# Optimization experiments

Hardware: AMD Instinct MI355X
Metric: run time of the kernel (lower is better)

## Reference

```python
import jax, jax.numpy as jnp
import numpy as np

DIM = 1024
DIM_HEAD = 64
HEADS = 8
INNER = DIM_HEAD * HEADS
EPS = 1e-5


def layernorm(x, g, b):
    mu = jnp.mean(x, axis=-1, keepdims=True)
    var = jnp.var(x, axis=-1, keepdims=True)
    return (x - mu) * jax.lax.rsqrt(var + EPS) * g + b


def setup_inputs() -> dict:
    key = jax.random.key(0)
    ks = jax.random.split(key, 8)
    b, n, m = 8, 4096, 64
    x = jax.random.normal(ks[0], (b, n, DIM), dtype=jnp.float32)
    latents = jax.random.normal(ks[1], (b, m, DIM), dtype=jnp.float32)
    mask = jax.random.bernoulli(ks[2], 0.9, (b, n))
    s = DIM ** -0.5
    Wq = jax.random.normal(ks[3], (DIM, INNER), dtype=jnp.float32) * s
    Wkv = jax.random.normal(ks[4], (DIM, 2 * INNER), dtype=jnp.float32) * s
    Wo = jax.random.normal(ks[5], (INNER, DIM), dtype=jnp.float32) * (INNER ** -0.5)
    ln_x_g = jnp.ones((DIM,), jnp.float32); ln_x_b = jnp.zeros((DIM,), jnp.float32)
    ln_l_g = jnp.ones((DIM,), jnp.float32); ln_l_b = jnp.zeros((DIM,), jnp.float32)
    ln_o_g = jnp.ones((DIM,), jnp.float32); ln_o_b = jnp.zeros((DIM,), jnp.float32)
    return {"x": x, "latents": latents, "mask": mask,
            "Wq": Wq, "Wkv": Wkv, "Wo": Wo,
            "ln_x_g": ln_x_g, "ln_x_b": ln_x_b,
            "ln_l_g": ln_l_g, "ln_l_b": ln_l_b,
            "ln_o_g": ln_o_g, "ln_o_b": ln_o_b}


def reference(x, latents, mask, Wq, Wkv, Wo, ln_x_g, ln_x_b, ln_l_g, ln_l_b, ln_o_g, ln_o_b):
    scale = DIM_HEAD ** -0.5
    b, m = latents.shape[0], latents.shape[1]
    xn = layernorm(x, ln_x_g, ln_x_b)
    ln = layernorm(latents, ln_l_g, ln_l_b)
    q = ln @ Wq                                   # [b, m, inner]
    kv_in = jnp.concatenate([xn, ln], axis=1)     # [b, n+m, dim]
    kv = kv_in @ Wkv                              # [b, n+m, 2*inner]
    k, v = jnp.split(kv, 2, axis=-1)
    # b n (h d) -> b h n d
    q = q.reshape(b, m, HEADS, DIM_HEAD).transpose(0, 2, 1, 3)
    k = k.reshape(b, k.shape[1], HEADS, DIM_HEAD).transpose(0, 2, 1, 3)
    v = v.reshape(b, v.shape[1], HEADS, DIM_HEAD).transpose(0, 2, 1, 3)
    # NOTE: scale applied twice, faithful to the original module.
    sim = jnp.einsum('bhid,bhjd->bhij', q * scale, k) * scale
    full_mask = jnp.concatenate([mask, jnp.ones((b, m), dtype=bool)], axis=1)  # pad True for latents
    max_neg = -jnp.finfo(sim.dtype).max
    sim = jnp.where(full_mask[:, None, None, :], sim, max_neg)
    attn = jax.nn.softmax(sim.astype(jnp.float32), axis=-1).astype(sim.dtype)
    out = jnp.einsum('bhij,bhjd->bhid', attn, v)
    out = out.transpose(0, 2, 1, 3).reshape(b, m, INNER)
    out = out @ Wo
    return layernorm(out, ln_o_g, ln_o_b)
```

## Files before the change

### kernel.cpp

```cpp
#include <hip/hip_runtime.h>

typedef unsigned short u16;
typedef unsigned int u32;
using f32x4  = __attribute__((ext_vector_type(4))) float;
using short8 = __attribute__((ext_vector_type(8))) short;
using s16x4  = __attribute__((ext_vector_type(4))) short;
using u16x4  = __attribute__((ext_vector_type(4))) unsigned short;

#define DEV __device__ __forceinline__

DEV u16 f2bf(float f) {
  u32 u = __float_as_uint(f);
  u32 r = u + 0x7fffu + ((u >> 16) & 1u);
  return (u16)(r >> 16);
}

DEV void gload_lds16(const void* g, void* l) {
  __builtin_amdgcn_global_load_lds(
      (__attribute__((address_space(1))) void*)g,
      (__attribute__((address_space(3))) void*)l, 16, 0, 0);
}

DEV void block_reduce2(float& a, float& b, float* red) {
#pragma unroll
  for (int m = 1; m < 64; m <<= 1) {
    a += __shfl_xor(a, m);
    b += __shfl_xor(b, m);
  }
  const int wid = threadIdx.x >> 6, lane = threadIdx.x & 63;
  __syncthreads();
  if (lane == 0) { red[wid] = a; red[4 + wid] = b; }
  __syncthreads();
  a = red[0] + red[1] + red[2] + red[3];
  b = red[4] + red[5] + red[6] + red[7];
}

__global__ __launch_bounds__(256) void ln_rows_k(
    const float* __restrict__ X, const float* __restrict__ g,
    const float* __restrict__ be, u16* __restrict__ out, int mode)
{
  __shared__ float red[8];
  const int r = blockIdx.x, t = threadIdx.x;
  const float4 v = *(const float4*)(X + (((size_t)r) << 10) + t * 4);
  float s1 = v.x + v.y + v.z + v.w;
  float s2 = v.x * v.x + v.y * v.y + v.z * v.z + v.w * v.w;
  block_reduce2(s1, s2, red);
  const float mean = s1 * (1.f / 1024.f);
  const float var  = s2 * (1.f / 1024.f) - mean * mean;
  const float rstd = rsqrtf(var + 1e-5f);
  const float4 gv = *(const float4*)(g + t * 4);
  const float4 bv = *(const float4*)(be + t * 4);
  u16x4 o;
  o[0] = f2bf((v.x - mean) * rstd * gv.x + bv.x);
  o[1] = f2bf((v.y - mean) * rstd * gv.y + bv.y);
  o[2] = f2bf((v.z - mean) * rstd * gv.z + bv.z);
  o[3] = f2bf((v.w - mean) * rstd * gv.w + bv.w);
  const size_t orow = (mode == 0)
      ? ((size_t)(r >> 12) * 4160 + (r & 4095))
      : ((size_t)(r >> 6) * 4160 + 4096 + (r & 63));
  *(u16x4*)(out + orow * 1024 + t * 4) = o;
}

__global__ __launch_bounds__(256) void transpose_w_k(
    const float* __restrict__ W, u16* __restrict__ Wt, int K, int N)
{
  __shared__ float tile[32][33];
  const int n0 = blockIdx.x * 32, k0 = blockIdx.y * 32;
  const int tx = threadIdx.x, ty = threadIdx.y;
#pragma unroll
  for (int i = 0; i < 4; ++i)
    tile[ty + 8 * i][tx] = W[(size_t)(k0 + ty + 8 * i) * N + n0 + tx];
  __syncthreads();
#pragma unroll
  for (int i = 0; i < 4; ++i)
    Wt[(size_t)(n0 + ty + 8 * i) * K + k0 + tx] = f2bf(tile[tx][ty + 8 * i]);
}

__global__ __launch_bounds__(256) void mask_bias_k(const void* __restrict__ mask,
                                                   float* __restrict__ bias)
{
  __shared__ int flag_s;
  if (threadIdx.x == 0) {
    const u32* mw = (const u32*)mask;
    bool fpat = true, ipat = true;
    for (int i = 0; i < 256; ++i) {
      u32 w = mw[i];
      if (w != 0u && w != 0x3f800000u) fpat = false;
      if (w > 1u) ipat = false;
    }
    flag_s = fpat ? 2 : (ipat ? 1 : 0);
  }
  __syncthreads();
  const int flag = flag_s;
  const int idx = blockIdx.x * 256 + threadIdx.x;
  const int b = idx / 4160, j = idx - b * 4160;
  float bv = 0.f;
  if (j < 4096) {
    const int mi = b * 4096 + j;
    bool on;
    if (flag == 2)      on = ((const float*)mask)[mi] != 0.f;
    else if (flag == 1) on = ((const int*)mask)[mi] != 0;
    else                on = ((const unsigned char*)mask)[mi] != 0;
    bv = on ? 0.f : -1e30f;
  }
  bias[idx] = bv;
}

__global__ __launch_bounds__(512, 4) void gemm2_k(
    const u16* __restrict__ xnl, const u16* __restrict__ Wq_t,
    const u16* __restrict__ Wkv_t,
    u16* __restrict__ q_h, u16* __restrict__ k_h, u16* __restrict__ v_t)
{
  __shared__ __attribute__((aligned(16))) short As[3][4096];
  __shared__ __attribute__((aligned(16))) short Bs[3][8192];

  const int tid = threadIdx.x, lane = tid & 63;
  const int wid = tid >> 6, wr = wid >> 2, wc = wid & 3;
  const int l15 = lane & 15, lq = lane >> 4;

  const int bid = blockIdx.x;
  int mode, mblk, nblk;
  const u16 *Ap, *Bp;
  if (bid < 520)       { mode = 0; mblk = bid % 260; nblk = bid / 260; Ap = xnl; Bp = Wkv_t; }
  else if (bid < 1040) { const int r2 = bid - 520; mode = 2; mblk = r2 & 3; nblk = r2 >> 2;
                         Ap = Wkv_t + (size_t)512 * 1024; Bp = xnl; }
  else                 { const int r2 = bid - 1040; mode = 1; mblk = r2 >> 1; nblk = r2 & 1;
                         Ap = xnl; Bp = Wq_t; }
  const int m0 = mblk * 128, n0 = nblk * 256;

  const int srow = tid >> 2, sslot = tid & 3;
  const u32 ss = (u32)((sslot ^ ((srow >> 1) & 3)) * 8);
  const int gra = m0 + srow;
  const u32 arow = (mode == 1) ? ((u32)(gra >> 6) * 4160u + 4096u + (u32)(gra & 63)) : (u32)gra;
  const u32 aoff  = arow * 1024u + ss;
  const u32 boff0 = (u32)(n0 + srow) * 1024u + ss;
  const u32 boff1 = (u32)(n0 + 128 + srow) * 1024u + ss;

  const int rsw = ((lq ^ ((l15 >> 1) & 3)) << 4);
  const int aRd = wr * 4096 + l15 * 64 + rsw;
  const int bRd = wc * 4096 + l15 * 64 + rsw;

  const f32x4 z4 = {0.f, 0.f, 0.f, 0.f};
  f32x4 acc[4][4];
#pragma unroll
  for (int i = 0; i < 4; ++i)
#pragma unroll
    for (int j = 0; j < 4; ++j) acc[i][j] = z4;

  auto stage = [&](int buf, int T) {
    gload_lds16(Ap + aoff  + (u32)T * 32u, &As[buf][tid * 8]);
    gload_lds16(Bp + boff0 + (u32)T * 32u, &Bs[buf][tid * 8]);
    gload_lds16(Bp + boff1 + (u32)T * 32u, &Bs[buf][4096 + tid * 8]);
  };

  stage(0, 0);
  stage(1, 1);
  asm volatile("s_waitcnt vmcnt(3)" ::: "memory");
  __builtin_amdgcn_s_barrier();

  int c0 = 0, c1 = 1, c2 = 2;
#pragma unroll 1
  for (int t = 0; t < 32; ++t) {
    if (t < 30) stage(c2, t + 2);
    const char* aB = (const char*)&As[0][0] + c0 * 8192  + aRd;
    const char* bB = (const char*)&Bs[0][0] + c0 * 16384 + bRd;
    short8 af[4], bf[4];
#pragma unroll
    for (int mi = 0; mi < 4; ++mi) af[mi] = *(const short8*)(aB + mi * 1024);
#pragma unroll
    for (int nj = 0; nj < 4; ++nj) bf[nj] = *(const short8*)(bB + nj * 1024);
    __builtin_amdgcn_s_setprio(1);
#pragma unroll
    for (int mi = 0; mi < 4; ++mi)
#pragma unroll
      for (int nj = 0; nj < 4; ++nj)
        acc[mi][nj] = __builtin_amdgcn_mfma_f32_16x16x32_bf16(af[mi], bf[nj], acc[mi][nj], 0, 0, 0);
    __builtin_amdgcn_s_setprio(0);
    if (t < 30)       { asm volatile("s_waitcnt vmcnt(3)" ::: "memory"); }
    else if (t == 30) { asm volatile("s_waitcnt vmcnt(0)" ::: "memory"); }
    __builtin_amdgcn_s_barrier();
    const int tmp = c0; c0 = c1; c1 = c2; c2 = tmp;
  }

#pragma unroll
  for (int mi = 0; mi < 4; ++mi)
#pragma unroll
    for (int nj = 0; nj < 4; ++nj)
#pragma unroll
      for (int r = 0; r < 4; ++r) {
        const int gm = m0 + wr * 64 + mi * 16 + lq * 4 + r;
        const int gn = n0 + wc * 64 + nj * 16 + l15;
        const u16 v = f2bf(acc[mi][nj][r]);
        if (mode == 0) {
          const int b = gm / 4160, j = gm - b * 4160;
          k_h[(((size_t)b * 8 + (gn >> 6)) * 4160 + j) * 64 + (gn & 63)] = v;
        } else if (mode == 2) {
          const int b = gn / 4160, j = gn - b * 4160;
          v_t[(((size_t)b * 8 + (gm >> 6)) * 64 + (gm & 63)) * 4160 + j] = v;
        } else {
          const int b = gm >> 6, i2 = gm & 63;
          q_h[(((size_t)b * 8 + (gn >> 6)) * 64 + i2) * 64 + (gn & 63)] = v;
        }
      }
}

__global__ __launch_bounds__(256) void attn_k(
    const u16* __restrict__ q_h, const u16* __restrict__ k_h,
    const u16* __restrict__ v_t, const float* __restrict__ bias,
    float* __restrict__ O_part, float* __restrict__ m_part,
    float* __restrict__ l_part)
{
  __shared__ __attribute__((aligned(16))) short Ks[4096];
  __shared__ __attribute__((aligned(16))) short Vs[4096];
  __shared__ __attribute__((aligned(16))) short Ps[4][1152];
  __shared__ float biasS[64];
  const int bid = blockIdx.x;
  const int sp = bid & 7, bh = bid >> 3;
  const int b = bh >> 3;
  const int tid = threadIdx.x, wid = tid >> 6, lane = tid & 63;
  const int t0 = sp ? (8 * sp + 1) : 0;
  const int tc = sp ? 8 : 9;

  const size_t qoff = ((size_t)bh * 64 + wid * 16 + (lane & 15)) * 64 + 8 * (lane >> 4);
  const short8 qf0 = *(const short8*)&q_h[qoff];
  const short8 qf1 = *(const short8*)&q_h[qoff + 32];

  float mrun = -1e30f, lrun = 0.f;
  const f32x4 z4 = {0.f, 0.f, 0.f, 0.f};
  f32x4 o[4] = {z4, z4, z4, z4};
  const size_t khead = (size_t)bh * (4160 * 64);
  const size_t vhead = (size_t)bh * (64 * 4160);

  for (int tt = 0; tt < tc; ++tt) {
    const int t = t0 + tt;
#pragma unroll
    for (int p = 0; p < 2; ++p) {
      const int lo = (p * 256 + tid) * 16;
      const int row = lo >> 7;
      const int src = lo ^ ((row & 7) << 4);
      gload_lds16((const char*)k_h + (khead + (size_t)t * 4096) * 2 + src,
                  (char*)Ks + (p * 256 + wid * 64) * 16);
    }
#pragma unroll
    for (int p = 0; p < 2; ++p) {
      const int lo = (p * 256 + tid) * 16;
      const int row = lo >> 7;
      const int colb = (lo ^ ((row & 7) << 4)) & 127;
      gload_lds16((const char*)v_t + (vhead + (size_t)row * 4160 + t * 64) * 2 + colb,
                  (char*)Vs + (p * 256 + wid * 64) * 16);
    }
    if (tid < 64) biasS[tid] = bias[b * 4160 + t * 64 + tid];
    __syncthreads();

    f32x4 sc[4] = {z4, z4, z4, z4};
#pragma unroll
    for (int mi = 0; mi < 4; ++mi) {
      const int row = mi * 16 + (lane & 15);
      const int sw = (row & 7) << 4;
      short8 a0 = *(const short8*)((const char*)Ks + ((row * 128 + 16 * (lane >> 4)) ^ sw));
      sc[mi] = __builtin_amdgcn_mfma_f32_16x16x32_bf16(a0, qf0, sc[mi], 0, 0, 0);
      short8 a1 = *(const short8*)((const char*)Ks + ((row * 128 + 64 + 16 * (lane >> 4)) ^ sw));
      sc[mi] = __builtin_amdgcn_mfma_f32_16x16x32_bf16(a1, qf1, sc[mi], 0, 0, 0);
    }

    float sv[4][4];
    float tmax = -3e30f;
#pragma unroll
    for (int mi = 0; mi < 4; ++mi)
#pragma unroll
      for (int r = 0; r < 4; ++r) {
        const int kv = mi * 16 + (lane >> 4) * 4 + r;
        const float s = sc[mi][r] * (1.f / 64.f) + biasS[kv];
        sv[mi][r] = s;
        tmax = fmaxf(tmax, s);
      }
    tmax = fmaxf(tmax, __shfl_xor(tmax, 16));
    tmax = fmaxf(tmax, __shfl_xor(tmax, 32));
    const float mnew = fmaxf(mrun, tmax);
    const float fac = __expf(mrun - mnew);
    float psum = 0.f;
#pragma unroll
    for (int mi = 0; mi < 4; ++mi) {
      s16x4 pk;
#pragma unroll
      for (int r = 0; r < 4; ++r) {
        const float p = __expf(sv[mi][r] - mnew);
        psum += p;
        pk[r] = (short)f2bf(p);
      }
      *(s16x4*)&Ps[wid][(lane & 15) * 72 + mi * 16 + (lane >> 4) * 4] = pk;
    }
    psum += __shfl_xor(psum, 16);
    psum += __shfl_xor(psum, 32);
    lrun = lrun * fac + psum;
    mrun = mnew;
#pragma unroll
    for (int mi = 0; mi < 4; ++mi)
#pragma unroll
      for (int e = 0; e < 4; ++e) o[mi][e] *= fac;

#pragma unroll
    for (int mi = 0; mi < 4; ++mi) {
      const int row = mi * 16 + (lane & 15);
      const int sw = (row & 7) << 4;
      short8 a0 = *(const short8*)((const char*)Vs + ((row * 128 + 16 * (lane >> 4)) ^ sw));
      short8 p0 = *(const short8*)&Ps[wid][(lane & 15) * 72 + 8 * (lane >> 4)];
      o[mi] = __builtin_amdgcn_mfma_f32_16x16x32_bf16(a0, p0, o[mi], 0, 0, 0);
      short8 a1 = *(const short8*)((const char*)Vs + ((row * 128 + 64 + 16 * (lane >> 4)) ^ sw));
      short8 p1 = *(const short8*)&Ps[wid][(lane & 15) * 72 + 32 + 8 * (lane >> 4)];
      o[mi] = __builtin_amdgcn_mfma_f32_16x16x32_bf16(a1, p1, o[mi], 0, 0, 0);
    }
    __syncthreads();
  }

#pragma unroll
  for (int mi = 0; mi < 4; ++mi)
#pragma unroll
    for (int r = 0; r < 4; ++r) {
      const int d = mi * 16 + (lane >> 4) * 4 + r;
      const int q = wid * 16 + (lane & 15);
      O_part[(((size_t)sp * 64 + bh) * 64 + d) * 64 + q] = o[mi][r];
    }
  if (lane < 16) {
    m_part[((size_t)sp * 64 + bh) * 64 + wid * 16 + lane] = mrun;
    l_part[((size_t)sp * 64 + bh) * 64 + wid * 16 + lane] = lrun;
  }
}

__global__ __launch_bounds__(256) void combine_k(
    const float* __restrict__ O_part, const float* __restrict__ m_part,
    const float* __restrict__ l_part, float* __restrict__ attn_out)
{
  __shared__ float wgt[8][64];
  const int bh = blockIdx.x;
  const int b = bh >> 3, h = bh & 7;
  const int t = threadIdx.x;
  if (t < 64) {
    float mv[8], lv[8];
#pragma unroll
    for (int s = 0; s < 8; ++s) {
      mv[s] = m_part[((size_t)s * 64 + bh) * 64 + t];
      lv[s] = l_part[((size_t)s * 64 + bh) * 64 + t];
    }
    float M = mv[0];
#pragma unroll
    for (int s = 1; s < 8; ++s) M = fmaxf(M, mv[s]);
    float den = 0.f;
#pragma unroll
    for (int s = 0; s < 8; ++s) den += lv[s] * __expf(mv[s] - M);
    const float inv = 1.f / den;
#pragma unroll
    for (int s = 0; s < 8; ++s) wgt[s][t] = __expf(mv[s] - M) * inv;
  }
  __syncthreads();
#pragma unroll
  for (int i = 0; i < 16; ++i) {
    const int p = i * 256 + t;
    const int d = p >> 6, q = p & 63;
    float acc = 0.f;
#pragma unroll
    for (int s = 0; s < 8; ++s)
      acc += O_part[(((size_t)s * 64 + bh) * 64 + d) * 64 + q] * wgt[s][q];
    attn_out[((size_t)b * 64 + q) * 512 + h * 64 + d] = acc;
  }
}

__global__ __launch_bounds__(256) void outproj_k(
    const float* __restrict__ attn_out, const float* __restrict__ Wo,
    const float* __restrict__ g, const float* __restrict__ be,
    float* __restrict__ out)
{
  __shared__ float arow[2][512];
  __shared__ float red[8];
  const int rb = blockIdx.x * 2, t = threadIdx.x;
  arow[0][t]       = attn_out[(size_t)rb * 512 + t];
  arow[0][t + 256] = attn_out[(size_t)rb * 512 + 256 + t];
  arow[1][t]       = attn_out[(size_t)(rb + 1) * 512 + t];
  arow[1][t + 256] = attn_out[(size_t)(rb + 1) * 512 + 256 + t];
  __syncthreads();
  float a0x = 0, a0y = 0, a0z = 0, a0w = 0;
  float a1x = 0, a1y = 0, a1z = 0, a1w = 0;
  for (int k = 0; k < 512; ++k) {
    const float4 w = *(const float4*)(Wo + (size_t)k * 1024 + t * 4);
    const float x0 = arow[0][k], x1 = arow[1][k];
    a0x += x0 * w.x; a0y += x0 * w.y; a0z += x0 * w.z; a0w += x0 * w.w;
    a1x += x1 * w.x; a1y += x1 * w.y; a1z += x1 * w.z; a1w += x1 * w.w;
  }
  const float4 gv = *(const float4*)(g + t * 4);
  const float4 bv = *(const float4*)(be + t * 4);
  {
    float s1 = a0x + a0y + a0z + a0w;
    float s2 = a0x * a0x + a0y * a0y + a0z * a0z + a0w * a0w;
    block_reduce2(s1, s2, red);
    const float mean = s1 * (1.f / 1024.f);
    const float rstd = rsqrtf(s2 * (1.f / 1024.f) - mean * mean + 1e-5f);
    float4 ov;
    ov.x = (a0x - mean) * rstd * gv.x + bv.x;
    ov.y = (a0y - mean) * rstd * gv.y + bv.y;
    ov.z = (a0z - mean) * rstd * gv.z + bv.z;
    ov.w = (a0w - mean) * rstd * gv.w + bv.w;
    *(float4*)(out + (size_t)rb * 1024 + t * 4) = ov;
  }
  {
    float s1 = a1x + a1y + a1z + a1w;
    float s2 = a1x * a1x + a1y * a1y + a1z * a1z + a1w * a1w;
    block_reduce2(s1, s2, red);
    const float mean = s1 * (1.f / 1024.f);
    const float rstd = rsqrtf(s2 * (1.f / 1024.f) - mean * mean + 1e-5f);
    float4 ov;
    ov.x = (a1x - mean) * rstd * gv.x + bv.x;
    ov.y = (a1y - mean) * rstd * gv.y + bv.y;
    ov.z = (a1z - mean) * rstd * gv.z + bv.z;
    ov.w = (a1w - mean) * rstd * gv.w + bv.w;
    *(float4*)(out + (size_t)(rb + 1) * 1024 + t * 4) = ov;
  }
}

extern "C" void kernel_launch(void* const* d_in, const int* in_sizes, int n_in,
                              void* d_out, int out_size, void* d_ws, size_t ws_size,
                              hipStream_t stream) {
  (void)in_sizes; (void)n_in; (void)out_size; (void)ws_size;
  const float* x       = (const float*)d_in[0];
  const float* latents = (const float*)d_in[1];
  const void*  mask    = d_in[2];
  const float* Wq      = (const float*)d_in[3];
  const float* Wkv     = (const float*)d_in[4];
  const float* Wo      = (const float*)d_in[5];
  const float* gx      = (const float*)d_in[6];
  const float* bx      = (const float*)d_in[7];
  const float* gl      = (const float*)d_in[8];
  const float* bl      = (const float*)d_in[9];
  const float* go      = (const float*)d_in[10];
  const float* bo      = (const float*)d_in[11];
  float* out = (float*)d_out;

  char* w = (char*)d_ws;
  u16* xnl   = (u16*)w; w += (size_t)33280 * 1024 * 2;
  u16* Wq_t  = (u16*)w; w += (size_t)512 * 1024 * 2;
  u16* Wkv_t = (u16*)w; w += (size_t)1024 * 1024 * 2;
  u16* q_h   = (u16*)w; w += (size_t)8 * 8 * 64 * 64 * 2;
  u16* k_h   = (u16*)w; w += (size_t)8 * 8 * 4160 * 64 * 2;
  u16* v_t   = (u16*)w; w += (size_t)8 * 8 * 64 * 4160 * 2;
  float* bias   = (float*)w; w += (size_t)8 * 4160 * 4;
  float* O_part = (float*)w; w += (size_t)8 * 64 * 64 * 64 * 4;
  float* m_part = (float*)w; w += (size_t)8 * 64 * 64 * 4;
  float* l_part = (float*)w; w += (size_t)8 * 64 * 64 * 4;
  float* attnO  = (float*)w; w += (size_t)512 * 512 * 4;

  transpose_w_k<<<dim3(16, 32), dim3(32, 8), 0, stream>>>(Wq, Wq_t, 1024, 512);
  transpose_w_k<<<dim3(32, 32), dim3(32, 8), 0, stream>>>(Wkv, Wkv_t, 1024, 1024);
  ln_rows_k<<<dim3(32768), dim3(256), 0, stream>>>(x, gx, bx, xnl, 0);
  ln_rows_k<<<dim3(512), dim3(256), 0, stream>>>(latents, gl, bl, xnl, 1);
  mask_bias_k<<<dim3(130), dim3(256), 0, stream>>>(mask, bias);
  gemm2_k<<<dim3(1048), dim3(512), 0, stream>>>(xnl, Wq_t, Wkv_t, q_h, k_h, v_t);
  attn_k<<<dim3(512), dim3(256), 0, stream>>>(q_h, k_h, v_t, bias, O_part, m_part, l_part);
  combine_k<<<dim3(64), dim3(256), 0, stream>>>(O_part, m_part, l_part, attnO);
  outproj_k<<<dim3(256), dim3(256), 0, stream>>>(attnO, Wo, go, bo, out);
}
```

Measured before the change: 245.1 us.

## Enlarge projection GEMM tiles to 256x256 with a persistent job loop

The fused Q/K/V projection GEMM now computes 256x256 output tiles instead of 128x256, giving each wave an 8x4 MFMA accumulator block. It launches 512 blocks that loop over 524 jobs, aiming for more data reuse per LDS load and fewer tile reloads. The price is doubled A-tile LDS, lower occupancy (launch bounds 2), and higher register pressure. The XOR LDS swizzle is also dropped, which may cause bank conflicts, and 12 jobs spill into a second pass as a tail.

```diff
diff --git a/kernel.cpp b/kernel.cpp
--- a/kernel.cpp
+++ b/kernel.cpp
@@ -106,102 +106,104 @@
   bias[idx] = bv;
 }
 
-__global__ __launch_bounds__(512, 4) void gemm2_k(
+__global__ __launch_bounds__(512, 2) void gemm3_k(
     const u16* __restrict__ xnl, const u16* __restrict__ Wq_t,
     const u16* __restrict__ Wkv_t,
     u16* __restrict__ q_h, u16* __restrict__ k_h, u16* __restrict__ v_t)
 {
-  __shared__ __attribute__((aligned(16))) short As[3][4096];
+  __shared__ __attribute__((aligned(16))) short As[3][8192];
   __shared__ __attribute__((aligned(16))) short Bs[3][8192];
 
   const int tid = threadIdx.x, lane = tid & 63;
   const int wid = tid >> 6, wr = wid >> 2, wc = wid & 3;
   const int l15 = lane & 15, lq = lane >> 4;
 
-  const int bid = blockIdx.x;
-  int mode, mblk, nblk;
-  const u16 *Ap, *Bp;
-  if (bid < 520)       { mode = 0; mblk = bid % 260; nblk = bid / 260; Ap = xnl; Bp = Wkv_t; }
-  else if (bid < 1040) { const int r2 = bid - 520; mode = 2; mblk = r2 & 3; nblk = r2 >> 2;
-                         Ap = Wkv_t + (size_t)512 * 1024; Bp = xnl; }
-  else                 { const int r2 = bid - 1040; mode = 1; mblk = r2 >> 1; nblk = r2 & 1;
-                         Ap = xnl; Bp = Wq_t; }
-  const int m0 = mblk * 128, n0 = nblk * 256;
-
-  const int srow = tid >> 2, sslot = tid & 3;
-  const u32 ss = (u32)((sslot ^ ((srow >> 1) & 3)) * 8);
-  const int gra = m0 + srow;
-  const u32 arow = (mode == 1) ? ((u32)(gra >> 6) * 4160u + 4096u + (u32)(gra & 63)) : (u32)gra;
-  const u32 aoff  = arow * 1024u + ss;
-  const u32 boff0 = (u32)(n0 + srow) * 1024u + ss;
-  const u32 boff1 = (u32)(n0 + 128 + srow) * 1024u + ss;
-
-  const int rsw = ((lq ^ ((l15 >> 1) & 3)) << 4);
-  const int aRd = wr * 4096 + l15 * 64 + rsw;
-  const int bRd = wc * 4096 + l15 * 64 + rsw;
-
-  const f32x4 z4 = {0.f, 0.f, 0.f, 0.f};
-  f32x4 acc[4][4];
-#pragma unroll
-  for (int i = 0; i < 4; ++i)
-#pragma unroll
-    for (int j = 0; j < 4; ++j) acc[i][j] = z4;
-
-  auto stage = [&](int buf, int T) {
-    gload_lds16(Ap + aoff  + (u32)T * 32u, &As[buf][tid * 8]);
-    gload_lds16(Bp + boff0 + (u32)T * 32u, &Bs[buf][tid * 8]);
-    gload_lds16(Bp + boff1 + (u32)T * 32u, &Bs[buf][4096 + tid * 8]);
-  };
-
-  stage(0, 0);
-  stage(1, 1);
-  asm volatile("s_waitcnt vmcnt(3)" ::: "memory");
-  __builtin_amdgcn_s_barrier();
-
-  int c0 = 0, c1 = 1, c2 = 2;
+  const int aRd = (wr * 128 + l15) * 32 + lq * 8;
+  const int bRd = (wc * 64 + l15) * 32 + lq * 8;
+
+  for (u32 job = blockIdx.x; job < 524; job += 512) {
+    int mode, mblk, nblk;
+    const u16 *Ap, *Bp;
+    if (job < 260)      { mode = 0; mblk = job % 130; nblk = job / 130; Ap = xnl; Bp = Wkv_t; }
+    else if (job < 520) { const int r2 = job - 260; mode = 2; mblk = r2 & 1; nblk = r2 >> 1;
+                          Ap = Wkv_t + (size_t)512 * 1024; Bp = xnl; }
+    else                { const int r2 = job - 520; mode = 1; mblk = r2 & 1; nblk = r2 >> 1;
+                          Ap = xnl; Bp = Wq_t; }
+    const int m0 = mblk * 256, n0 = nblk * 256;
+
+    const int srow = tid >> 2, sslot = tid & 3;
+    const int gra0 = m0 + srow, gra1 = m0 + 128 + srow;
+    const u32 ar0 = (mode == 1) ? ((u32)(gra0 >> 6) * 4160u + 4096u + (u32)(gra0 & 63)) : (u32)gra0;
+    const u32 ar1 = (mode == 1) ? ((u32)(gra1 >> 6) * 4160u + 4096u + (u32)(gra1 & 63)) : (u32)gra1;
+    const u32 asrc0 = ar0 * 1024u + (u32)sslot * 8u;
+    const u32 asrc1 = ar1 * 1024u + (u32)sslot * 8u;
+    const u32 bsrc0 = (u32)(n0 + srow) * 1024u + (u32)sslot * 8u;
+    const u32 bsrc1 = (u32)(n0 + 128 + srow) * 1024u + (u32)sslot * 8u;
+
+    const f32x4 z4 = {0.f, 0.f, 0.f, 0.f};
+    f32x4 acc[8][4];
+#pragma unroll
+    for (int i = 0; i < 8; ++i)
+#pragma unroll
+      for (int j = 0; j < 4; ++j) acc[i][j] = z4;
+
+    auto stage = [&](int buf, int T) {
+      gload_lds16(Ap + asrc0 + (u32)T * 32u, &As[buf][tid * 8]);
+      gload_lds16(Ap + asrc1 + (u32)T * 32u, &As[buf][4096 + tid * 8]);
+      gload_lds16(Bp + bsrc0 + (u32)T * 32u, &Bs[buf][tid * 8]);
+      gload_lds16(Bp + bsrc1 + (u32)T * 32u, &Bs[buf][4096 + tid * 8]);
+    };
+
+    stage(0, 0);
+    stage(1, 1);
+    asm volatile("s_waitcnt vmcnt(4)" ::: "memory");
+    __builtin_amdgcn_s_barrier();
+
+    int c0 = 0, c1 = 1, c2 = 2;
 #pragma unroll 1
-  for (int t = 0; t < 32; ++t) {
-    if (t < 30) stage(c2, t + 2);
-    const char* aB = (const char*)&As[0][0] + c0 * 8192  + aRd;
-    const char* bB = (const char*)&Bs[0][0] + c0 * 16384 + bRd;
-    short8 af[4], bf[4];
-#pragma unroll
-    for (int mi = 0; mi < 4; ++mi) af[mi] = *(const short8*)(aB + mi * 1024);
-#pragma unroll
-    for (int nj = 0; nj < 4; ++nj) bf[nj] = *(const short8*)(bB + nj * 1024);
-    __builtin_amdgcn_s_setprio(1);
-#pragma unroll
-    for (int mi = 0; mi < 4; ++mi)
+    for (int t = 0; t < 32; ++t) {
+      if (t < 30) stage(c2, t + 2);
+      const short* aB = &As[0][0] + c0 * 8192 + aRd;
+      const short* bB = &Bs[0][0] + c0 * 8192 + bRd;
+      short8 af[8], bf[4];
+#pragma unroll
+      for (int mi = 0; mi < 8; ++mi) af[mi] = *(const short8*)(aB + mi * 512);
+#pragma unroll
+      for (int nj = 0; nj < 4; ++nj) bf[nj] = *(const short8*)(bB + nj * 512);
+      __builtin_amdgcn_s_setprio(1);
+#pragma unroll
+      for (int mi = 0; mi < 8; ++mi)
+#pragma unroll
+        for (int nj = 0; nj < 4; ++nj)
+          acc[mi][nj] = __builtin_amdgcn_mfma_f32_16x16x32_bf16(af[mi], bf[nj], acc[mi][nj], 0, 0, 0);
+      __builtin_amdgcn_s_setprio(0);
+      if (t < 30)       { asm volatile("s_waitcnt vmcnt(4)" ::: "memory"); }
+      else if (t == 30) { asm volatile("s_waitcnt vmcnt(0)" ::: "memory"); }
+      __builtin_amdgcn_s_barrier();
+      const int tmp = c0; c0 = c1; c1 = c2; c2 = tmp;
+    }
+
+#pragma unroll
+    for (int mi = 0; mi < 8; ++mi)
 #pragma unroll
       for (int nj = 0; nj < 4; ++nj)
-        acc[mi][nj] = __builtin_amdgcn_mfma_f32_16x16x32_bf16(af[mi], bf[nj], acc[mi][nj], 0, 0, 0);
-    __builtin_amdgcn_s_setprio(0);
-    if (t < 30)       { asm volatile("s_waitcnt vmcnt(3)" ::: "memory"); }
-    else if (t == 30) { asm volatile("s_waitcnt vmcnt(0)" ::: "memory"); }
-    __builtin_amdgcn_s_barrier();
-    const int tmp = c0; c0 = c1; c1 = c2; c2 = tmp;
-  }
-
-#pragma unroll
-  for (int mi = 0; mi < 4; ++mi)
-#pragma unroll
-    for (int nj = 0; nj < 4; ++nj)
-#pragma unroll
-      for (int r = 0; r < 4; ++r) {
-        const int gm = m0 + wr * 64 + mi * 16 + lq * 4 + r;
-        const int gn = n0 + wc * 64 + nj * 16 + l15;
-        const u16 v = f2bf(acc[mi][nj][r]);
-        if (mode == 0) {
-          const int b = gm / 4160, j = gm - b * 4160;
-          k_h[(((size_t)b * 8 + (gn >> 6)) * 4160 + j) * 64 + (gn & 63)] = v;
-        } else if (mode == 2) {
-          const int b = gn / 4160, j = gn - b * 4160;
-          v_t[(((size_t)b * 8 + (gm >> 6)) * 64 + (gm & 63)) * 4160 + j] = v;
-        } else {
-          const int b = gm >> 6, i2 = gm & 63;
-          q_h[(((size_t)b * 8 + (gn >> 6)) * 64 + i2) * 64 + (gn & 63)] = v;
+#pragma unroll
+        for (int r = 0; r < 4; ++r) {
+          const int gm = m0 + wr * 128 + mi * 16 + lq * 4 + r;
+          const int gn = n0 + wc * 64 + nj * 16 + l15;
+          const u16 v = f2bf(acc[mi][nj][r]);
+          if (mode == 0) {
+            const int b = gm / 4160, j = gm - b * 4160;
+            k_h[(((size_t)b * 8 + (gn >> 6)) * 4160 + j) * 64 + (gn & 63)] = v;
+          } else if (mode == 2) {
+            const int b = gn / 4160, j = gn - b * 4160;
+            v_t[(((size_t)b * 8 + (gm >> 6)) * 64 + (gm & 63)) * 4160 + j] = v;
+          } else {
+            const int b = gm >> 6, i2 = gm & 63;
+            q_h[(((size_t)b * 8 + (gn >> 6)) * 64 + i2) * 64 + (gn & 63)] = v;
+          }
         }
-      }
+  }
 }
 
 __global__ __launch_bounds__(256) void attn_k(
@@ -452,7 +454,7 @@
   ln_rows_k<<<dim3(32768), dim3(256), 0, stream>>>(x, gx, bx, xnl, 0);
   ln_rows_k<<<dim3(512), dim3(256), 0, stream>>>(latents, gl, bl, xnl, 1);
   mask_bias_k<<<dim3(130), dim3(256), 0, stream>>>(mask, bias);
-  gemm2_k<<<dim3(1048), dim3(512), 0, stream>>>(xnl, Wq_t, Wkv_t, q_h, k_h, v_t);
+  gemm3_k<<<dim3(512), dim3(512), 0, stream>>>(xnl, Wq_t, Wkv_t, q_h, k_h, v_t);
   attn_k<<<dim3(512), dim3(256), 0, stream>>>(q_h, k_h, v_t, bias, O_part, m_part, l_part);
   combine_k<<<dim3(64), dim3(256), 0, stream>>>(O_part, m_part, l_part, attnO);
   outproj_k<<<dim3(256), dim3(256), 0, stream>>>(attnO, Wo, go, bo, out);
```

After: 272.7 us. 1.11x slower.
